# Performance work log

Measured on AMD Instinct MI355X. Metric: run time of the kernel, lower is better.

The kernel has to match this reference:

```python
import jax, jax.numpy as jnp
from jax import lax
import numpy as np


def _conv(x, w, b, pad):
    y = lax.conv_general_dilated(x, w, (1, 1), [(pad, pad), (pad, pad)],
                                 dimension_numbers=('NCHW', 'OIHW', 'NCHW'))
    return y + b[None, :, None, None]


def _bn(x, g, b, eps=1e-5):
    # training-mode batchnorm (batch statistics, biased variance) like torch default
    m = jnp.mean(x, (0, 2, 3), keepdims=True)
    v = jnp.mean((x - m) ** 2, (0, 2, 3), keepdims=True)
    return g[None, :, None, None] * (x - m) * lax.rsqrt(v + eps) + b[None, :, None, None]


def _maxpool2(x):
    return lax.reduce_window(x, -jnp.inf, lax.max, (1, 1, 2, 2), (1, 1, 2, 2), 'VALID')


def _power_features(x):
    # vectorized version of the per-image FFT + radial-bin histogram mean
    B, _, H, W = x.shape
    cy, cx = H // 2, W // 2
    yy, xx = jnp.meshgrid(jnp.arange(H), jnp.arange(W), indexing='ij')
    r = jnp.sqrt((xx - cx).astype(jnp.float32) ** 2 + (yy - cy).astype(jnp.float32) ** 2)
    max_r = min(H, W) // 2
    NB = 32
    r_bins = jnp.linspace(0.0, float(max_r), NB + 1)
    # bin j covers [r_bins[j], r_bins[j+1]) exactly as the torch mask
    idx = jnp.searchsorted(r_bins, r.ravel(), side='right') - 1
    valid = (idx >= 0) & (idx < NB)
    seg = jnp.where(valid, idx, NB)  # dump out-of-range into bin NB
    counts = jax.ops.segment_sum(valid.astype(jnp.float32), seg, NB + 1)[:NB]
    ps = jnp.abs(jnp.fft.fft2(x[:, 0])) ** 2  # [B,H,W]
    psf = ps.reshape(B, -1) * valid.astype(ps.dtype)[None, :]
    sums = jax.vmap(lambda p: jax.ops.segment_sum(p, seg, NB + 1))(psf)[:, :NB]
    radial = jnp.where(counts > 0, sums / jnp.maximum(counts, 1.0), 0.0)
    return jnp.log(radial + 1e-10)  # [B,32]


def reference(x, cw1, cb1, g1, bb1, cw2, cb2, g2, bb2, cw3, cb3, g3, bb3,
              cw4, cb4, g4, bb4, pcw, pcb, pg, pbb,
              pw1, pb1, pw2, pb2, pw3, pb3,
              fw1, fb1, fw2, fb2, fw3, fb3, fw4, fb4):
    h = jax.nn.relu(_bn(_conv(x, cw1, cb1, 2), g1, bb1)); h = _maxpool2(h)
    h = jax.nn.relu(_bn(_conv(h, cw2, cb2, 2), g2, bb2)); h = _maxpool2(h)
    h = jax.nn.relu(_bn(_conv(h, cw3, cb3, 1), g3, bb3)); h = _maxpool2(h)
    h = jax.nn.relu(_bn(_conv(h, cw4, cb4, 1), g4, bb4))        # [B,256,32,32]
    p = jax.nn.relu(_bn(_conv(h, pcw, pcb, 1), pg, pbb))        # [B,128,32,32]
    # adaptive avg pool (4,4): exact 8x8 windows, stride 8
    p = lax.reduce_window(p, 0.0, lax.add, (1, 1, 8, 8), (1, 1, 8, 8), 'VALID') / 64.0
    flat = p.reshape(p.shape[0], -1)  # [B,2048]
    pf = _power_features(x)           # [B,32]
    pf = jax.nn.relu(pf @ pw1.T + pb1)
    pf = jax.nn.relu(pf @ pw2.T + pb2)
    pf = jax.nn.relu(pf @ pw3.T + pb3)  # [B,64]
    c = jnp.concatenate([flat, pf], axis=1)  # [B,2112]
    c = jax.nn.relu(c @ fw1.T + fb1)
    c = jax.nn.relu(c @ fw2.T + fb2)
    c = jax.nn.relu(c @ fw3.T + fb3)
    return c @ fw4.T + fb4  # [B,2]


def setup_inputs() -> dict:
    key = jax.random.key(0)
    ki = iter(jax.random.split(key, 40))

    def W(shape):
        fan_in = int(np.prod(shape[1:]))
        return jax.random.normal(next(ki), shape, jnp.float32) / np.sqrt(fan_in)

    d = {'x': jax.random.normal(next(ki), (16, 1, 256, 256), jnp.float32)}
    convs = [('cw1', 'cb1', 'g1', 'bb1', (32, 1, 5, 5)),
             ('cw2', 'cb2', 'g2', 'bb2', (64, 32, 5, 5)),
             ('cw3', 'cb3', 'g3', 'bb3', (128, 64, 3, 3)),
             ('cw4', 'cb4', 'g4', 'bb4', (256, 128, 3, 3)),
             ('pcw', 'pcb', 'pg', 'pbb', (128, 256, 3, 3))]
    for wn, bn, gn, ben, s in convs:
        d[wn] = W(s); d[bn] = jnp.zeros(s[0], jnp.float32)
        d[gn] = jnp.ones(s[0], jnp.float32); d[ben] = jnp.zeros(s[0], jnp.float32)
    lins = [('pw1', 'pb1', (256, 32)), ('pw2', 'pb2', (128, 256)), ('pw3', 'pb3', (64, 128)),
            ('fw1', 'fb1', (512, 2112)), ('fw2', 'fb2', (256, 512)),
            ('fw3', 'fb3', (128, 256)), ('fw4', 'fb4', (2, 128))]
    for wn, bn, s in lins:
        d[wn] = W(s); d[bn] = jnp.zeros(s[0], jnp.float32)
    return d
```

## Files before the change

kernel.cpp:

```cpp
#include <hip/hip_runtime.h>
#include <math.h>


#define PI2F 6.283185307179586f

typedef _Float16 half8 __attribute__((ext_vector_type(8)));
typedef _Float16 half4v __attribute__((ext_vector_type(4)));
typedef float f32x4 __attribute__((ext_vector_type(4)));


__device__ __forceinline__ int bitrev8(int x) {
  x = ((x & 0x0F) << 4) | ((x >> 4) & 0x0F);
  x = ((x & 0x33) << 2) | ((x >> 2) & 0x33);
  x = ((x & 0x55) << 1) | ((x >> 1) & 0x55);
  return x;
}

__global__ __launch_bounds__(64)
void fft_rows(const float* __restrict__ x, float2* __restrict__ out) {
  __shared__ float2 s[256];
  __shared__ float2 tw[128];
  int blk = blockIdx.x;
  const float* rowp = x + (size_t)blk * 256;
  int t = threadIdx.x;
  for (int i = t; i < 128; i += 64) {
    float sn, cs;
    sincosf(-(PI2F / 256.f) * (float)i, &sn, &cs);
    tw[i] = make_float2(cs, sn);
  }
  #pragma unroll
  for (int e = 0; e < 4; ++e) {
    int i = t + (e << 6);
    s[bitrev8(i)] = make_float2(rowp[i], 0.f);
  }
  __syncthreads();
  #pragma unroll
  for (int st = 1; st <= 8; ++st) {
    int half = 1 << (st - 1);
    #pragma unroll
    for (int j = 0; j < 2; ++j) {
      int bf = t + (j << 6);
      int pos = bf & (half - 1);
      int grp = bf >> (st - 1);
      int i0 = (grp << st) | pos;
      int i1 = i0 + half;
      int k = pos << (8 - st);
      float cs = tw[k].x, sn = tw[k].y;
      float2 a = s[i0], b = s[i1];
      float tr = cs * b.x - sn * b.y;
      float ti = cs * b.y + sn * b.x;
      s[i0] = make_float2(a.x + tr, a.y + ti);
      s[i1] = make_float2(a.x - tr, a.y - ti);
    }
    __syncthreads();
  }
  float2* op = out + (size_t)blk * 256;
  #pragma unroll
  for (int e = 0; e < 4; ++e) { int i = t + (e << 6); op[i] = s[i]; }
}

__device__ __forceinline__ int radial_bin(int r2) {
  int j = (int)(sqrtf((float)r2) * 0.25f);
  while ((j + 1) * (j + 1) * 16 <= r2) ++j;
  while (j > 0 && j * j * 16 > r2) --j;
  return j;
}

__global__ __launch_bounds__(256)
void fft_cols_radial_v2(const float2* __restrict__ f, float* __restrict__ radial) {
  __shared__ float2 s[8][258];
  __shared__ float2 tw[128];
  __shared__ float bins[8][32];
  int b = blockIdx.x >> 5;
  int col0 = (blockIdx.x & 31) * 8;
  int t = threadIdx.x;
  for (int i = t; i < 128; i += 256) {
    float sn, cs;
    sincosf(-(PI2F / 256.f) * (float)i, &sn, &cs);
    tw[i] = make_float2(cs, sn);
  }
  ((float*)bins)[t] = 0.f;
  for (int idx = t; idx < 2048; idx += 256) {
    int row = idx >> 3, c = idx & 7;
    s[c][bitrev8(row)] = f[(size_t)b * 65536 + row * 256 + col0 + c];
  }
  __syncthreads();
  int c = t >> 5, l = t & 31;
  float2* sc = &s[c][0];
  #pragma unroll
  for (int st = 1; st <= 8; ++st) {
    int half = 1 << (st - 1);
    #pragma unroll
    for (int j = 0; j < 4; ++j) {
      int bf = l + (j << 5);
      int pos = bf & (half - 1);
      int grp = bf >> (st - 1);
      int i0 = (grp << st) | pos;
      int i1 = i0 + half;
      int k = pos << (8 - st);
      float cs = tw[k].x, sn = tw[k].y;
      float2 a = sc[i0], bb = sc[i1];
      float tr = cs * bb.x - sn * bb.y;
      float ti = cs * bb.y + sn * bb.x;
      sc[i0] = make_float2(a.x + tr, a.y + ti);
      sc[i1] = make_float2(a.x - tr, a.y - ti);
    }
    __syncthreads();
  }
  int dx = col0 + c - 128;
  #pragma unroll
  for (int e = 0; e < 8; ++e) {
    int i = l * 8 + e;
    float2 v = sc[i];
    float ps = v.x * v.x + v.y * v.y;
    int dy = i - 128;
    int r2 = dx * dx + dy * dy;
    if (r2 < 16384) atomicAdd(&bins[c][radial_bin(r2)], ps);
  }
  __syncthreads();
  if (t < 32) {
    float s0 = bins[0][t] + bins[1][t] + bins[2][t] + bins[3][t] +
               bins[4][t] + bins[5][t] + bins[6][t] + bins[7][t];
    atomicAdd(&radial[b * 32 + t], s0);
  }
}

__device__ __forceinline__ int isqrt_(int v) {
  int r = (int)sqrtf((float)v);
  while (r * r > v) --r;
  while ((r + 1) * (r + 1) <= v) ++r;
  return r;
}

__global__ __launch_bounds__(256)
void radial_finalize_v3(const float* __restrict__ radial, float* __restrict__ pf0) {
  __shared__ int red[4];
  __shared__ int cnt_s;
  int j = blockIdx.x, t = threadIdx.x;
  int dy = t - 128;
  int lo = 16 * j * j, hi = 16 * (j + 1) * (j + 1);
  int d2 = dy * dy;
  int cnt = 0;
  int tHi = hi - 1 - d2;
  if (tHi >= 0) {
    int rHi = isqrt_(tHi);
    int nHi = min(rHi, 127) + min(rHi, 128) + 1;
    int nLo = 0;
    int tLo = lo - 1 - d2;
    if (tLo >= 0) { int rLo = isqrt_(tLo); nLo = min(rLo, 127) + min(rLo, 128) + 1; }
    cnt = nHi - nLo;
  }
  #pragma unroll
  for (int off = 32; off > 0; off >>= 1) cnt += __shfl_down(cnt, off);
  if ((t & 63) == 0) red[t >> 6] = cnt;
  __syncthreads();
  if (t == 0) cnt_s = red[0] + red[1] + red[2] + red[3];
  __syncthreads();
  if (t < 16) {
    float cf = (float)cnt_s;
    float sum = radial[t * 32 + j];
    float val = cf > 0.f ? sum / fmaxf(cf, 1.f) : 0.f;
    pf0[t * 32 + j] = logf(val + 1e-10f);
  }
}


__global__ __launch_bounds__(256)
void wtrans_all(const float* __restrict__ cw2, const float* __restrict__ cw3,
                const float* __restrict__ cw4, const float* __restrict__ pcw,
                _Float16* __restrict__ wb2, _Float16* __restrict__ wb3,
                _Float16* __restrict__ wb4, _Float16* __restrict__ wbp) {
  int blk = blockIdx.x;
  const float* src; _Float16* dst; int COUT, CIN, KK, i;
  if (blk < 200)       { src = cw2; dst = wb2; COUT = 64;  CIN = 32;  KK = 25; i = blk * 256; }
  else if (blk < 488)  { src = cw3; dst = wb3; COUT = 128; CIN = 64;  KK = 9;  i = (blk - 200) * 256; }
  else if (blk < 1640) { src = cw4; dst = wb4; COUT = 256; CIN = 128; KK = 9;  i = (blk - 488) * 256; }
  else                 { src = pcw; dst = wbp; COUT = 128; CIN = 256; KK = 9;  i = (blk - 1640) * 256; }
  i += threadIdx.x;
  if (i >= COUT * CIN * KK) return;
  int ci = i % CIN;
  int r = i / CIN;
  int co = r % COUT;
  int tap = r / COUT;
  dst[i] = (_Float16)src[((size_t)co * CIN + ci) * KK + tap];
}


__device__ __forceinline__ void load16(float* d, const float* p) {
  f32x4 v0 = *(const f32x4*)(p);
  f32x4 v1 = *(const f32x4*)(p + 4);
  f32x4 v2 = *(const f32x4*)(p + 8);
  f32x4 v3 = *(const f32x4*)(p + 12);
  #pragma unroll
  for (int e = 0; e < 4; ++e) { d[e] = v0[e]; d[4+e] = v1[e]; d[8+e] = v2[e]; d[12+e] = v3[e]; }
}

__global__ __launch_bounds__(256)
void conv1_fused(const float* __restrict__ x, const float* __restrict__ w,
                 _Float16* __restrict__ praw, size_t minoff,
                 float* __restrict__ stats) {
  __shared__ float lds[8 * 264];
  __shared__ float r1[4][32], r2[4][32];
  int t = threadIdx.x;
  int y0 = blockIdx.x * 4, n = blockIdx.y;
  const float* xp = x + (size_t)n * 65536;
  for (int i = t; i < 8 * 264; i += 256) {
    int r = i / 264, cc = i % 264;
    int gy = y0 + r - 2, gx = cc - 4;
    lds[i] = (gy >= 0 && gy < 256 && gx >= 0 && gx < 256) ? xp[gy * 256 + gx] : 0.f;
  }
  __syncthreads();
  int c = t & 31, xg = t >> 5;
  float wreg[25];
  #pragma unroll
  for (int k = 0; k < 25; ++k) wreg[k] = w[c * 25 + k];
  float s1 = 0.f, s2 = 0.f;
  for (int strip = 0; strip < 4; ++strip) {
    int px0 = xg * 8 + strip * 64;
    float f[5][16];
    #pragma unroll
    for (int rr = 0; rr < 4; ++rr) load16(f[rr], &lds[rr * 264 + px0]);
    float pmax[4], pmin[4];
    #pragma unroll
    for (int r = 0; r < 4; ++r) {
      load16(f[(r + 4) % 5], &lds[(r + 4) * 264 + px0]);
      f32x4 A = {0.f, 0.f, 0.f, 0.f}, B = {0.f, 0.f, 0.f, 0.f};
      #pragma unroll
      for (int ky = 0; ky < 5; ++ky) {
        const float* fr = f[(r + ky) % 5];
        #pragma unroll
        for (int kx = 0; kx < 5; ++kx) {
          float wv = wreg[ky * 5 + kx];
          f32x4 ia = {fr[2 + kx], fr[3 + kx], fr[4 + kx], fr[5 + kx]};
          f32x4 ib = {fr[6 + kx], fr[7 + kx], fr[8 + kx], fr[9 + kx]};
          A += wv * ia; B += wv * ib;
        }
      }
      s1 += A[0] + A[1] + A[2] + A[3] + B[0] + B[1] + B[2] + B[3];
      s2 += A[0]*A[0] + A[1]*A[1] + A[2]*A[2] + A[3]*A[3]
          + B[0]*B[0] + B[1]*B[1] + B[2]*B[2] + B[3]*B[3];
      float cm[4], cn[4];
      cm[0] = fmaxf(A[0], A[1]); cn[0] = fminf(A[0], A[1]);
      cm[1] = fmaxf(A[2], A[3]); cn[1] = fminf(A[2], A[3]);
      cm[2] = fmaxf(B[0], B[1]); cn[2] = fminf(B[0], B[1]);
      cm[3] = fmaxf(B[2], B[3]); cn[3] = fminf(B[2], B[3]);
      if ((r & 1) == 0) {
        #pragma unroll
        for (int k = 0; k < 4; ++k) { pmax[k] = cm[k]; pmin[k] = cn[k]; }
      } else {
        int prow = (y0 + r) >> 1;
        int pc0 = px0 >> 1;
        #pragma unroll
        for (int k = 0; k < 4; ++k) {
          size_t idx = (((size_t)n * 128 + prow) * 128 + pc0 + k) * 32 + c;
          praw[idx] = (_Float16)fmaxf(pmax[k], cm[k]);
          praw[minoff + idx] = (_Float16)fminf(pmin[k], cn[k]);
        }
      }
    }
  }
  s1 += __shfl_down(s1, 32);
  s2 += __shfl_down(s2, 32);
  if ((t & 63) < 32) { r1[t >> 6][t & 31] = s1; r2[t >> 6][t & 31] = s2; }
  __syncthreads();
  if (t < 32) {
    float* st = stats + (blockIdx.x & 7) * 64;
    atomicAdd(&st[t],      r1[0][t] + r1[1][t] + r1[2][t] + r1[3][t]);
    atomicAdd(&st[32 + t], r2[0][t] + r2[1][t] + r2[2][t] + r2[3][t]);
  }
}


__global__ __launch_bounds__(256)
void bn_apply(const _Float16* __restrict__ raw, size_t minoff,
              const float* __restrict__ stats, const float* __restrict__ g,
              const float* __restrict__ bb, _Float16* __restrict__ out,
              int C, int HWC, float invN) {
  __shared__ float scs[64], shs[64];
  int t = threadIdx.x, n = blockIdx.y;
  for (int c = t; c < C; c += 256) {
    float s1 = 0.f, s2 = 0.f;
    #pragma unroll
    for (int s = 0; s < 8; ++s) {
      s1 += stats[s * 2 * C + c];
      s2 += stats[s * 2 * C + C + c];
    }
    float mean = s1 * invN;
    float var  = s2 * invN - mean * mean;
    float k = g[c] / sqrtf(var + 1e-5f);
    scs[c] = k; shs[c] = bb[c] - mean * k;
  }
  __syncthreads();
  size_t basei = (size_t)n * HWC;
  int nv = HWC >> 3;
  for (int i = blockIdx.x * 256 + t; i < nv; i += gridDim.x * 256) {
    size_t off = basei + ((size_t)i << 3);
    half8 vmx = *(const half8*)(raw + off);
    half8 vmn = *(const half8*)(raw + minoff + off);
    int ch = (i << 3) & (C - 1);
    half8 o;
    #pragma unroll
    for (int j = 0; j < 8; ++j) {
      float sc = scs[ch + j];
      float xv = sc >= 0.f ? (float)vmx[j] : (float)vmn[j];
      o[j] = (_Float16)fmaxf(sc * xv + shs[ch + j], 0.f);
    }
    *(half8*)(out + off) = o;
  }
}


template <int CIN, int COUT, int H, int W, int K, int TH, int TW, int CW,
          int COT, int PT, int SLAB, int APPLY, int INPOOL, int OUTPOOL>
__global__ __launch_bounds__(256)
void conv_mfma5(const _Float16* __restrict__ in, size_t in_minoff,
                const _Float16* __restrict__ wb,
                _Float16* __restrict__ out, size_t out_minoff,
                const float* __restrict__ instats, const float* __restrict__ ing,
                const float* __restrict__ inbb, float in_invN,
                float* __restrict__ stats) {
  constexpr int P = K / 2, R = TH + 2 * P, XW = TW + 2 * P, PIX = R * XW;
  constexpr int TAPS = K * K, CSP = SLAB + 8;
  constexpr int NCC = SLAB / 32, NPH = CIN / SLAB, SUBS = SLAB / 8;
  constexpr int PW = 4 / CW, COB = CW * 16 * COT;
  static_assert(TH * TW == PW * 16 * PT, "pos tile mismatch");
  static_assert(TW == 16, "row-per-fragment requires TW=16");
  static_assert(!OUTPOOL || (PT % 2 == 0), "pool needs even PT");
  __shared__ _Float16 lds[PIX * CSP];
  __shared__ float inscs[APPLY ? CIN : 8], inshs[APPLY ? CIN : 8];
  __shared__ float sst[2][COB];
  int t = threadIdx.x;
  int lane = t & 63, wv = t >> 6;
  int lane15 = lane & 15, quad = lane >> 4;
  constexpr int WT = W / TW;
  int x0 = (blockIdx.x % WT) * TW, y0 = (blockIdx.x / WT) * TH;
  int coB = blockIdx.y * COB;
  int nb = blockIdx.z;
  int co_off = (wv % CW) * (16 * COT);
  int rowbase = (wv / CW) * PT;

  for (int i = t; i < 2 * COB; i += 256) ((float*)sst)[i] = 0.f;
  if (APPLY) {
    for (int c = t; c < CIN; c += 256) {
      float s1 = 0.f, s2 = 0.f;
      #pragma unroll
      for (int s = 0; s < 8; ++s) {
        s1 += instats[s * 2 * CIN + c];
        s2 += instats[s * 2 * CIN + CIN + c];
      }
      float mean = s1 * in_invN;
      float var  = s2 * in_invN - mean * mean;
      float k = ing[c] / sqrtf(var + 1e-5f);
      inscs[c] = k; inshs[c] = inbb[c] - mean * k;
    }
    __syncthreads();
  }

  f32x4 acc[COT][PT];
  #pragma unroll
  for (int ct = 0; ct < COT; ++ct)
    #pragma unroll
    for (int pt = 0; pt < PT; ++pt)
      #pragma unroll
      for (int e = 0; e < 4; ++e) acc[ct][pt][e] = 0.f;

  int bbase[PT];
  #pragma unroll
  for (int pt = 0; pt < PT; ++pt)
    bbase[pt] = ((rowbase + pt) * XW + lane15) * CSP + quad * 8;
  const _Float16* aptr[COT];
  #pragma unroll
  for (int ct = 0; ct < COT; ++ct)
    aptr[ct] = wb + (size_t)(coB + co_off + ct * 16 + lane15) * CIN + quad * 8;

  const size_t ibase = (size_t)nb * H * W * CIN;

  #pragma unroll
  for (int ph = 0; ph < NPH; ++ph) {
    constexpr int ITEMS = PIX * SUBS;
    for (int i = t; i < ITEMS; i += 256) {
      int sub = i % SUBS, pix = i / SUBS;
      int r = pix / XW, xx = pix % XW;
      int gy = y0 + r - P, gx = x0 + xx - P;
      int ch = ph * SLAB + sub * 8;
      half8 v;
      #pragma unroll
      for (int j = 0; j < 8; ++j) v[j] = (_Float16)0.f;
      if (gy >= 0 && gy < H && gx >= 0 && gx < W) {
        size_t off = ibase + ((size_t)gy * W + gx) * CIN + ch;
        half8 vmx = *(const half8*)(in + off);
        if (!APPLY) {
          v = vmx;
        } else if (INPOOL) {
          half8 vmn = *(const half8*)(in + in_minoff + off);
          #pragma unroll
          for (int j = 0; j < 8; ++j) {
            float sc = inscs[ch + j];
            float xv = sc >= 0.f ? (float)vmx[j] : (float)vmn[j];
            v[j] = (_Float16)fmaxf(sc * xv + inshs[ch + j], 0.f);
          }
        } else {
          #pragma unroll
          for (int j = 0; j < 8; ++j) {
            float sc = inscs[ch + j];
            v[j] = (_Float16)fmaxf(sc * (float)vmx[j] + inshs[ch + j], 0.f);
          }
        }
      }
      *(half8*)(&lds[pix * CSP + sub * 8]) = v;
    }
    __syncthreads();
    #pragma unroll
    for (int cc = 0; cc < NCC; ++cc) {
      #pragma unroll
      for (int tap = 0; tap < TAPS; ++tap) {
        int ky = tap / K, kx = tap % K;
        half8 a[COT], b[PT];
        #pragma unroll
        for (int ct = 0; ct < COT; ++ct)
          a[ct] = *(const half8*)(aptr[ct] + (size_t)tap * COUT * CIN +
                                  ph * SLAB + cc * 32);
        #pragma unroll
        for (int pt = 0; pt < PT; ++pt)
          b[pt] = *(const half8*)(&lds[bbase[pt] + (ky * XW + kx) * CSP + cc * 32]);
        #pragma unroll
        for (int ct = 0; ct < COT; ++ct)
          #pragma unroll
          for (int pt = 0; pt < PT; ++pt)
            acc[ct][pt] = __builtin_amdgcn_mfma_f32_16x16x32_f16(
                a[ct], b[pt], acc[ct][pt], 0, 0, 0);
      }
    }
    if (ph + 1 < NPH) __syncthreads();
  }

  if (OUTPOOL) {
    #pragma unroll
    for (int ct = 0; ct < COT; ++ct)
      #pragma unroll
      for (int pp = 0; pp < PT; pp += 2) {
        half4v hmax, hmin;
        #pragma unroll
        for (int e = 0; e < 4; ++e) {
          float vmx = fmaxf(acc[ct][pp][e], acc[ct][pp + 1][e]);
          float vmn = fminf(acc[ct][pp][e], acc[ct][pp + 1][e]);
          float omx = fmaxf(vmx, __shfl_xor(vmx, 1));
          float omn = fminf(vmn, __shfl_xor(vmn, 1));
          hmax[e] = (_Float16)omx; hmin[e] = (_Float16)omn;
        }
        if ((lane15 & 1) == 0) {
          int co = coB + co_off + ct * 16 + quad * 4;
          int prow = (y0 + rowbase + pp) >> 1;
          int pcol = (x0 >> 1) + (lane15 >> 1);
          size_t idx = (((size_t)nb * (H / 2) + prow) * (W / 2) + pcol) * COUT + co;
          *(half4v*)(out + idx) = hmax;
          *(half4v*)(out + out_minoff + idx) = hmin;
        }
      }
  } else {
    #pragma unroll
    for (int ct = 0; ct < COT; ++ct)
      #pragma unroll
      for (int pt = 0; pt < PT; ++pt) {
        int co = coB + co_off + ct * 16 + quad * 4;
        int y = y0 + rowbase + pt, x = x0 + lane15;
        _Float16* op = out + (((size_t)nb * H + y) * W + x) * COUT + co;
        half4v h;
        #pragma unroll
        for (int e = 0; e < 4; ++e) h[e] = (_Float16)acc[ct][pt][e];
        *(half4v*)op = h;
      }
  }

  #pragma unroll
  for (int ct = 0; ct < COT; ++ct)
    #pragma unroll
    for (int e = 0; e < 4; ++e) {
      float sv = 0.f, sq = 0.f;
      #pragma unroll
      for (int pt = 0; pt < PT; ++pt) {
        float v = acc[ct][pt][e];
        sv += v; sq += v * v;
      }
      sv += __shfl_xor(sv, 1); sq += __shfl_xor(sq, 1);
      sv += __shfl_xor(sv, 2); sq += __shfl_xor(sq, 2);
      sv += __shfl_xor(sv, 4); sq += __shfl_xor(sq, 4);
      sv += __shfl_xor(sv, 8); sq += __shfl_xor(sq, 8);
      if (lane15 == 0) {
        int cl = co_off + ct * 16 + quad * 4 + e;
        atomicAdd(&sst[0][cl], sv);
        atomicAdd(&sst[1][cl], sq);
      }
    }
  __syncthreads();
  float* st = stats + (blockIdx.x & 7) * 2 * COUT;
  for (int i = t; i < COB; i += 256) {
    atomicAdd(&st[coB + i], sst[0][i]);
    atomicAdd(&st[COUT + coB + i], sst[1][i]);
  }
}


__global__ __launch_bounds__(256)
void bn_avgpool_concat(const _Float16* __restrict__ x, const float* __restrict__ stats,
                       const float* __restrict__ g, const float* __restrict__ bb,
                       float* __restrict__ concat, float invN) {
  __shared__ float scs[128], shs[128];
  int t = threadIdx.x;
  int n = blockIdx.y;
  for (int c = t; c < 128; c += 256) {
    float s1 = 0.f, s2 = 0.f;
    #pragma unroll
    for (int s = 0; s < 8; ++s) {
      s1 += stats[s * 256 + c];
      s2 += stats[s * 256 + 128 + c];
    }
    float mean = s1 * invN;
    float var  = s2 * invN - mean * mean;
    float k = g[c] / sqrtf(var + 1e-5f);
    scs[c] = k; shs[c] = bb[c] - mean * k;
  }
  __syncthreads();
  int i = blockIdx.x * 256 + t;
  int c = i & 127, opix = i >> 7;
  int py = opix >> 2, px = opix & 3;
  float sc = scs[c], sh = shs[c];
  float s = 0.f;
  for (int yy = 0; yy < 8; ++yy)
    #pragma unroll
    for (int xx = 0; xx < 8; ++xx)
      s += fmaxf((float)x[(((size_t)n * 32 + py * 8 + yy) * 32 + px * 8 + xx) * 128 + c] * sc + sh, 0.f);
  concat[(size_t)n * 2112 + c * 16 + opix] = s * (1.f / 64.f);
}


__global__ __launch_bounds__(64)
void linear_k(const float* __restrict__ in, const float* __restrict__ w,
              const float* __restrict__ bias, float* __restrict__ out,
              int I, int in_stride, int out_stride, int relu) {
  int o = blockIdx.x, b = blockIdx.y;
  int lane = threadIdx.x;
  const float* ip = in + (size_t)b * in_stride;
  const float* wp = w + (size_t)o * I;
  float acc = 0.f;
  for (int i = lane; i < I; i += 64) acc += ip[i] * wp[i];
  #pragma unroll
  for (int off = 32; off > 0; off >>= 1) acc += __shfl_down(acc, off);
  if (lane == 0) {
    float v = acc + bias[o];
    if (relu) v = fmaxf(v, 0.f);
    out[(size_t)b * out_stride + o] = v;
  }
}

__global__ __launch_bounds__(256)
void pf_mlp(const float* __restrict__ pf0,
            const float* __restrict__ pw1, const float* __restrict__ pb1,
            const float* __restrict__ pw2, const float* __restrict__ pb2,
            const float* __restrict__ pw3, const float* __restrict__ pb3,
            float* __restrict__ concat) {
  __shared__ float a0[32], a1[256], a2[128];
  int b = blockIdx.x, t = threadIdx.x;
  if (t < 32) a0[t] = pf0[b * 32 + t];
  __syncthreads();
  {
    float s = pb1[t];
    for (int i = 0; i < 32; ++i) s += pw1[t * 32 + i] * a0[i];
    a1[t] = fmaxf(s, 0.f);
  }
  __syncthreads();
  if (t < 128) {
    float s = pb2[t];
    for (int i = 0; i < 256; ++i) s += pw2[t * 256 + i] * a1[i];
    a2[t] = fmaxf(s, 0.f);
  }
  __syncthreads();
  if (t < 64) {
    float s = pb3[t];
    for (int i = 0; i < 128; ++i) s += pw3[t * 128 + i] * a2[i];
    concat[(size_t)b * 2112 + 2048 + t] = fmaxf(s, 0.f);
  }
}

__global__ __launch_bounds__(256)
void fc_tail(const float* __restrict__ fc1o,
             const float* __restrict__ fw2, const float* __restrict__ fb2,
             const float* __restrict__ fw3, const float* __restrict__ fb3,
             const float* __restrict__ fw4, const float* __restrict__ fb4,
             float* __restrict__ out) {
  __shared__ float a1[512], a2[256], a3[128];
  int b = blockIdx.x, t = threadIdx.x;
  a1[t] = fc1o[b * 512 + t];
  a1[t + 256] = fc1o[b * 512 + t + 256];
  __syncthreads();
  {
    float s = fb2[t];
    for (int i = 0; i < 512; ++i) s += fw2[t * 512 + i] * a1[i];
    a2[t] = fmaxf(s, 0.f);
  }
  __syncthreads();
  if (t < 128) {
    float s = fb3[t];
    for (int i = 0; i < 256; ++i) s += fw3[t * 256 + i] * a2[i];
    a3[t] = fmaxf(s, 0.f);
  }
  __syncthreads();
  if (t < 2) {
    float s = fb4[t];
    for (int i = 0; i < 128; ++i) s += fw4[t * 128 + i] * a3[i];
    out[b * 2 + t] = s;
  }
}


extern "C" void kernel_launch(void* const* d_in, const int* in_sizes, int n_in,
                              void* d_out, int out_size, void* d_ws, size_t ws_size,
                              hipStream_t stream) {
  (void)in_sizes; (void)n_in; (void)out_size; (void)ws_size;
  const float* x   = (const float*)d_in[0];
  const float* cw1 = (const float*)d_in[1];
  const float* g1  = (const float*)d_in[3];
  const float* bb1 = (const float*)d_in[4];
  const float* cw2 = (const float*)d_in[5];
  const float* g2  = (const float*)d_in[7];
  const float* bb2 = (const float*)d_in[8];
  const float* cw3 = (const float*)d_in[9];
  const float* g3  = (const float*)d_in[11];
  const float* bb3 = (const float*)d_in[12];
  const float* cw4 = (const float*)d_in[13];
  const float* g4  = (const float*)d_in[15];
  const float* bb4 = (const float*)d_in[16];
  const float* pcw = (const float*)d_in[17];
  const float* pg  = (const float*)d_in[19];
  const float* pbb = (const float*)d_in[20];
  const float* pw1 = (const float*)d_in[21];
  const float* pb1 = (const float*)d_in[22];
  const float* pw2 = (const float*)d_in[23];
  const float* pb2 = (const float*)d_in[24];
  const float* pw3 = (const float*)d_in[25];
  const float* pb3 = (const float*)d_in[26];
  const float* fw1 = (const float*)d_in[27];
  const float* fb1 = (const float*)d_in[28];
  const float* fw2 = (const float*)d_in[29];
  const float* fb2 = (const float*)d_in[30];
  const float* fw3 = (const float*)d_in[31];
  const float* fb3 = (const float*)d_in[32];
  const float* fw4 = (const float*)d_in[33];
  const float* fb4 = (const float*)d_in[34];

  char* base = (char*)d_ws;
  float2*   fftbuf   = (float2*)(base + 0);
  _Float16* pool1raw = (_Float16*)(base + 0);
  _Float16* pool1app = (_Float16*)(base + 33554432);
  _Float16* pool2raw = (_Float16*)(base + 0);
  _Float16* pool2app = (_Float16*)(base + 16777216);
  _Float16* pool3raw = (_Float16*)(base + 0);
  _Float16* conv4raw = (_Float16*)(base + 8388608);
  _Float16* pconvo   = (_Float16*)(base + 16777216);
  _Float16* wb2      = (_Float16*)(base + 50331648);
  _Float16* wb3      = (_Float16*)(base + 50434048);
  _Float16* wb4      = (_Float16*)(base + 50581504);
  _Float16* wbp      = (_Float16*)(base + 51171328);
  float*    zbase    = (float*)(base + 51761152);
  float*    stats1   = zbase;
  float*    stats2   = zbase + 512;
  float*    stats3   = zbase + 1536;
  float*    stats4   = zbase + 3584;
  float*    stats5   = zbase + 7680;
  float*    radial   = zbase + 9728;
  float*    pf0      = (float*)(base + 51802112);
  float*    concat   = (float*)(base + 51804160);
  float*    fc1o     = (float*)(base + 51939328);

  hipMemsetAsync(zbase, 0, 10240 * sizeof(float), stream);

  wtrans_all<<<2792, 256, 0, stream>>>(cw2, cw3, cw4, pcw, wb2, wb3, wb4, wbp);

  fft_rows<<<4096, 64, 0, stream>>>(x, fftbuf);
  fft_cols_radial_v2<<<512, 256, 0, stream>>>(fftbuf, radial);
  radial_finalize_v3<<<32, 256, 0, stream>>>(radial, pf0);
  pf_mlp<<<16, 256, 0, stream>>>(pf0, pw1, pb1, pw2, pb2, pw3, pb3, concat);

  conv1_fused<<<dim3(64, 16), 256, 0, stream>>>(x, cw1, pool1raw, 8388608, stats1);
  bn_apply<<<dim3(128, 16), 256, 0, stream>>>(
      pool1raw, 8388608, stats1, g1, bb1, pool1app, 32, 524288, 1.f / 1048576.f);

  conv_mfma5<32, 64, 128, 128, 5, 4, 16, 2, 2, 2, 32, 0, 0, 1>
      <<<dim3(256, 1, 16), 256, 0, stream>>>(
      pool1app, 0, wb2, pool2raw, 4194304,
      nullptr, nullptr, nullptr, 0.f, stats2);
  bn_apply<<<dim3(128, 16), 256, 0, stream>>>(
      pool2raw, 4194304, stats2, g2, bb2, pool2app, 64, 262144, 1.f / 262144.f);

  conv_mfma5<64, 128, 64, 64, 3, 4, 16, 2, 2, 2, 64, 0, 0, 1>
      <<<dim3(64, 2, 16), 256, 0, stream>>>(
      pool2app, 0, wb3, pool3raw, 2097152,
      nullptr, nullptr, nullptr, 0.f, stats3);

  conv_mfma5<128, 256, 32, 32, 3, 4, 16, 2, 2, 2, 128, 1, 1, 0>
      <<<dim3(16, 4, 16), 256, 0, stream>>>(
      pool3raw, 2097152, wb4, conv4raw, 0,
      stats3, g3, bb3, 1.f / 65536.f, stats4);

  conv_mfma5<256, 128, 32, 32, 3, 4, 16, 2, 2, 2, 128, 1, 0, 0>
      <<<dim3(16, 2, 16), 256, 0, stream>>>(
      conv4raw, 0, wbp, pconvo, 0,
      stats4, g4, bb4, 1.f / 16384.f, stats5);
  bn_avgpool_concat<<<dim3(8, 16), 256, 0, stream>>>(
      pconvo, stats5, pg, pbb, concat, 1.f / 16384.f);

  linear_k<<<dim3(512, 16), 64, 0, stream>>>(concat, fw1, fb1, fc1o, 2112, 2112, 512, 1);
  fc_tail<<<16, 256, 0, stream>>>(fc1o, fw2, fb2, fw3, fb3, fw4, fb4, (float*)d_out);
}
```

Baseline: 434.0 us.

## Use 32x32 MFMA for conv2/conv3 and split stats, BN+pool into passes

Adds a conv kernel built on the 32x32x16 MFMA instruction for conv2 and conv3. It writes full-resolution fp16 outputs with no fused pooling or statistics. A separate stats_pass computes the batchnorm sums, and a new bn_applypool kernel fuses BN, ReLU and 2x2 max-pool, replacing the earlier max/min dual-buffer pooling scheme. Conv4 now reads the already-normalized pooled input instead of applying BN on the fly. The larger MFMA tiles are meant to raise matrix throughput, but the change adds extra full-resolution memory traffic and more kernel launches.

```diff
diff --git a/kernel.cpp b/kernel.cpp
--- a/kernel.cpp
+++ b/kernel.cpp
@@ -7,6 +7,7 @@
 typedef _Float16 half8 __attribute__((ext_vector_type(8)));
 typedef _Float16 half4v __attribute__((ext_vector_type(4)));
 typedef float f32x4 __attribute__((ext_vector_type(4)));
+typedef float f32x16 __attribute__((ext_vector_type(16)));
 
 
 __device__ __forceinline__ int bitrev8(int x) {
@@ -271,6 +272,21 @@
 }
 
 
+__device__ __forceinline__ void bn_coeff(const float* stats, int C, int c,
+                                         float invN, const float* g,
+                                         const float* bb, float* sc, float* sh) {
+  float s1 = 0.f, s2 = 0.f;
+  #pragma unroll
+  for (int s = 0; s < 8; ++s) {
+    s1 += stats[s * 2 * C + c];
+    s2 += stats[s * 2 * C + C + c];
+  }
+  float mean = s1 * invN;
+  float var  = s2 * invN - mean * mean;
+  float k = g[c] / sqrtf(var + 1e-5f);
+  *sc = k; *sh = bb[c] - mean * k;
+}
+
 __global__ __launch_bounds__(256)
 void bn_apply(const _Float16* __restrict__ raw, size_t minoff,
               const float* __restrict__ stats, const float* __restrict__ g,
@@ -278,18 +294,7 @@
               int C, int HWC, float invN) {
   __shared__ float scs[64], shs[64];
   int t = threadIdx.x, n = blockIdx.y;
-  for (int c = t; c < C; c += 256) {
-    float s1 = 0.f, s2 = 0.f;
-    #pragma unroll
-    for (int s = 0; s < 8; ++s) {
-      s1 += stats[s * 2 * C + c];
-      s2 += stats[s * 2 * C + C + c];
-    }
-    float mean = s1 * invN;
-    float var  = s2 * invN - mean * mean;
-    float k = g[c] / sqrtf(var + 1e-5f);
-    scs[c] = k; shs[c] = bb[c] - mean * k;
-  }
+  for (int c = t; c < C; c += 256) bn_coeff(stats, C, c, invN, g, bb, &scs[c], &shs[c]);
   __syncthreads();
   size_t basei = (size_t)n * HWC;
   int nv = HWC >> 3;
@@ -306,6 +311,163 @@
       o[j] = (_Float16)fmaxf(sc * xv + shs[ch + j], 0.f);
     }
     *(half8*)(out + off) = o;
+  }
+}
+
+
+template <int CIN, int COUT, int H, int W, int K, int COT, int SLAB>
+__global__ __launch_bounds__(256)
+void conv_mfma32(const _Float16* __restrict__ in, const _Float16* __restrict__ wb,
+                 _Float16* __restrict__ out) {
+  constexpr int P = K / 2, TH = 8, TW = 16, R = TH + 2 * P, XW = TW + 2 * P;
+  constexpr int PIX = R * XW, TAPS = K * K, CSP = SLAB + 8;
+  constexpr int NCC = SLAB / 16, NPH = CIN / SLAB, SUBS = SLAB / 8;
+  constexpr int COB = 32 * COT;
+  __shared__ _Float16 lds[PIX * CSP];
+  int t = threadIdx.x;
+  int lane = t & 63, wv = t >> 6;
+  int n31 = lane & 31, khalf = lane >> 5;
+  constexpr int WT = W / TW;
+  int x0 = (blockIdx.x % WT) * TW, y0 = (blockIdx.x / WT) * TH;
+  int coB = blockIdx.y * COB;
+  int nb = blockIdx.z;
+  int rowbase = wv * 2;
+
+  f32x16 acc[COT];
+  #pragma unroll
+  for (int ct = 0; ct < COT; ++ct)
+    #pragma unroll
+    for (int e = 0; e < 16; ++e) acc[ct][e] = 0.f;
+
+  int bbase = ((rowbase + (n31 >> 4)) * XW + (n31 & 15)) * CSP + khalf * 8;
+  const _Float16* aptr[COT];
+  #pragma unroll
+  for (int ct = 0; ct < COT; ++ct)
+    aptr[ct] = wb + (size_t)(coB + ct * 32 + n31) * CIN + khalf * 8;
+
+  const size_t ibase = (size_t)nb * H * W * CIN;
+
+  #pragma unroll
+  for (int ph = 0; ph < NPH; ++ph) {
+    constexpr int ITEMS = PIX * SUBS;
+    for (int i = t; i < ITEMS; i += 256) {
+      int sub = i % SUBS, pix = i / SUBS;
+      int r = pix / XW, xx = pix % XW;
+      int gy = y0 + r - P, gx = x0 + xx - P;
+      half8 v;
+      #pragma unroll
+      for (int j = 0; j < 8; ++j) v[j] = (_Float16)0.f;
+      if (gy >= 0 && gy < H && gx >= 0 && gx < W)
+        v = *(const half8*)(in + ibase + ((size_t)gy * W + gx) * CIN +
+                            ph * SLAB + sub * 8);
+      *(half8*)(&lds[pix * CSP + sub * 8]) = v;
+    }
+    __syncthreads();
+    #pragma unroll
+    for (int cc = 0; cc < NCC; ++cc) {
+      #pragma unroll
+      for (int tap = 0; tap < TAPS; ++tap) {
+        int ky = tap / K, kx = tap % K;
+        half8 b = *(const half8*)(&lds[bbase + (ky * XW + kx) * CSP + cc * 16]);
+        #pragma unroll
+        for (int ct = 0; ct < COT; ++ct) {
+          half8 a = *(const half8*)(aptr[ct] + (size_t)tap * COUT * CIN +
+                                    ph * SLAB + cc * 16);
+          acc[ct] = __builtin_amdgcn_mfma_f32_32x32x16_f16(a, b, acc[ct], 0, 0, 0);
+        }
+      }
+    }
+    if (ph + 1 < NPH) __syncthreads();
+  }
+
+  int y = y0 + rowbase + (n31 >> 4), x = x0 + (n31 & 15);
+  _Float16* op = out + (((size_t)nb * H + y) * W + x) * COUT;
+  #pragma unroll
+  for (int ct = 0; ct < COT; ++ct)
+    #pragma unroll
+    for (int g = 0; g < 4; ++g) {
+      half4v h;
+      #pragma unroll
+      for (int e = 0; e < 4; ++e) h[e] = (_Float16)acc[ct][g * 4 + e];
+      *(half4v*)(op + coB + ct * 32 + 8 * g + 4 * khalf) = h;
+    }
+}
+
+
+template <int C>
+__global__ __launch_bounds__(256)
+void stats_pass(const _Float16* __restrict__ x, float* __restrict__ stats,
+                int HW) {
+  constexpr int CT = C / 8;
+  constexpr int PPB = 256 / CT;
+  __shared__ float red[256][16];
+  int t = threadIdx.x, n = blockIdx.y;
+  int cb = (t % CT) * 8, pr = t / CT;
+  int chunk = HW / 8;
+  int p0 = blockIdx.x * chunk;
+  float s[8], q[8];
+  #pragma unroll
+  for (int j = 0; j < 8; ++j) { s[j] = 0.f; q[j] = 0.f; }
+  const _Float16* xp = x + (size_t)n * HW * C;
+  for (int p = p0 + pr; p < p0 + chunk; p += PPB) {
+    half8 v = *(const half8*)(xp + (size_t)p * C + cb);
+    #pragma unroll
+    for (int j = 0; j < 8; ++j) { float f = (float)v[j]; s[j] += f; q[j] += f * f; }
+  }
+  #pragma unroll
+  for (int j = 0; j < 8; ++j) { red[t][j] = s[j]; red[t][8 + j] = q[j]; }
+  __syncthreads();
+  for (int st = 128; st >= CT; st >>= 1) {
+    if (t < st)
+      #pragma unroll
+      for (int j = 0; j < 16; ++j) red[t][j] += red[t + st][j];
+    __syncthreads();
+  }
+  if (t < CT) {
+    float* sl = stats + (blockIdx.x & 7) * 2 * C;
+    #pragma unroll
+    for (int j = 0; j < 8; ++j) {
+      atomicAdd(&sl[t * 8 + j], red[t][j]);
+      atomicAdd(&sl[C + t * 8 + j], red[t][8 + j]);
+    }
+  }
+}
+
+
+template <int C>
+__global__ __launch_bounds__(256)
+void bn_applypool(const _Float16* __restrict__ raw, const float* __restrict__ stats,
+                  const float* __restrict__ g, const float* __restrict__ bb,
+                  _Float16* __restrict__ out, int H, int W, float invN) {
+  constexpr int CT = C / 8;
+  __shared__ float scs[C], shs[C];
+  int t = threadIdx.x, n = blockIdx.y;
+  for (int c = t; c < C; c += 256) bn_coeff(stats, C, c, invN, g, bb, &scs[c], &shs[c]);
+  __syncthreads();
+  int W2 = W >> 1, H2 = H >> 1;
+  int total = H2 * W2 * CT;
+  const _Float16* xp = raw + (size_t)n * H * W * C;
+  _Float16* op = out + (size_t)n * H2 * W2 * C;
+  for (int i = blockIdx.x * 256 + t; i < total; i += gridDim.x * 256) {
+    int cb = (i % CT) * 8;
+    int pp = i / CT;
+    int py = pp / W2, px = pp % W2;
+    const _Float16* p00 = xp + ((size_t)(2 * py) * W + 2 * px) * C + cb;
+    half8 v00 = *(const half8*)(p00);
+    half8 v01 = *(const half8*)(p00 + C);
+    half8 v10 = *(const half8*)(p00 + (size_t)W * C);
+    half8 v11 = *(const half8*)(p00 + (size_t)W * C + C);
+    half8 o;
+    #pragma unroll
+    for (int j = 0; j < 8; ++j) {
+      float sc = scs[cb + j], sh = shs[cb + j];
+      float a = fmaxf(sc * (float)v00[j] + sh, 0.f);
+      float b = fmaxf(sc * (float)v01[j] + sh, 0.f);
+      float d = fmaxf(sc * (float)v10[j] + sh, 0.f);
+      float e = fmaxf(sc * (float)v11[j] + sh, 0.f);
+      o[j] = (_Float16)fmaxf(fmaxf(a, b), fmaxf(d, e));
+    }
+    *(half8*)(op + (size_t)pp * C + cb) = o;
   }
 }
 
@@ -325,7 +487,6 @@
   constexpr int PW = 4 / CW, COB = CW * 16 * COT;
   static_assert(TH * TW == PW * 16 * PT, "pos tile mismatch");
   static_assert(TW == 16, "row-per-fragment requires TW=16");
-  static_assert(!OUTPOOL || (PT % 2 == 0), "pool needs even PT");
   __shared__ _Float16 lds[PIX * CSP];
   __shared__ float inscs[APPLY ? CIN : 8], inshs[APPLY ? CIN : 8];
   __shared__ float sst[2][COB];
@@ -341,18 +502,8 @@
 
   for (int i = t; i < 2 * COB; i += 256) ((float*)sst)[i] = 0.f;
   if (APPLY) {
-    for (int c = t; c < CIN; c += 256) {
-      float s1 = 0.f, s2 = 0.f;
-      #pragma unroll
-      for (int s = 0; s < 8; ++s) {
-        s1 += instats[s * 2 * CIN + c];
-        s2 += instats[s * 2 * CIN + CIN + c];
-      }
-      float mean = s1 * in_invN;
-      float var  = s2 * in_invN - mean * mean;
-      float k = ing[c] / sqrtf(var + 1e-5f);
-      inscs[c] = k; inshs[c] = inbb[c] - mean * k;
-    }
+    for (int c = t; c < CIN; c += 256)
+      bn_coeff(instats, CIN, c, in_invN, ing, inbb, &inscs[c], &inshs[c]);
     __syncthreads();
   }
 
@@ -434,43 +585,18 @@
     if (ph + 1 < NPH) __syncthreads();
   }
 
-  if (OUTPOOL) {
-    #pragma unroll
-    for (int ct = 0; ct < COT; ++ct)
-      #pragma unroll
-      for (int pp = 0; pp < PT; pp += 2) {
-        half4v hmax, hmin;
-        #pragma unroll
-        for (int e = 0; e < 4; ++e) {
-          float vmx = fmaxf(acc[ct][pp][e], acc[ct][pp + 1][e]);
-          float vmn = fminf(acc[ct][pp][e], acc[ct][pp + 1][e]);
-          float omx = fmaxf(vmx, __shfl_xor(vmx, 1));
-          float omn = fminf(vmn, __shfl_xor(vmn, 1));
-          hmax[e] = (_Float16)omx; hmin[e] = (_Float16)omn;
-        }
-        if ((lane15 & 1) == 0) {
-          int co = coB + co_off + ct * 16 + quad * 4;
-          int prow = (y0 + rowbase + pp) >> 1;
-          int pcol = (x0 >> 1) + (lane15 >> 1);
-          size_t idx = (((size_t)nb * (H / 2) + prow) * (W / 2) + pcol) * COUT + co;
-          *(half4v*)(out + idx) = hmax;
-          *(half4v*)(out + out_minoff + idx) = hmin;
-        }
-      }
-  } else {
-    #pragma unroll
-    for (int ct = 0; ct < COT; ++ct)
-      #pragma unroll
-      for (int pt = 0; pt < PT; ++pt) {
-        int co = coB + co_off + ct * 16 + quad * 4;
-        int y = y0 + rowbase + pt, x = x0 + lane15;
-        _Float16* op = out + (((size_t)nb * H + y) * W + x) * COUT + co;
-        half4v h;
-        #pragma unroll
-        for (int e = 0; e < 4; ++e) h[e] = (_Float16)acc[ct][pt][e];
-        *(half4v*)op = h;
-      }
-  }
+  #pragma unroll
+  for (int ct = 0; ct < COT; ++ct)
+    #pragma unroll
+    for (int pt = 0; pt < PT; ++pt) {
+      int co = coB + co_off + ct * 16 + quad * 4;
+      int y = y0 + rowbase + pt, x = x0 + lane15;
+      _Float16* op = out + (((size_t)nb * H + y) * W + x) * COUT + co;
+      half4v h;
+      #pragma unroll
+      for (int e = 0; e < 4; ++e) h[e] = (_Float16)acc[ct][pt][e];
+      *(half4v*)op = h;
+    }
 
   #pragma unroll
   for (int ct = 0; ct < COT; ++ct)
@@ -508,18 +634,7 @@
   __shared__ float scs[128], shs[128];
   int t = threadIdx.x;
   int n = blockIdx.y;
-  for (int c = t; c < 128; c += 256) {
-    float s1 = 0.f, s2 = 0.f;
-    #pragma unroll
-    for (int s = 0; s < 8; ++s) {
-      s1 += stats[s * 256 + c];
-      s2 += stats[s * 256 + 128 + c];
-    }
-    float mean = s1 * invN;
-    float var  = s2 * invN - mean * mean;
-    float k = g[c] / sqrtf(var + 1e-5f);
-    scs[c] = k; shs[c] = bb[c] - mean * k;
-  }
+  for (int c = t; c < 128; c += 256) bn_coeff(stats, 128, c, invN, g, bb, &scs[c], &shs[c]);
   __syncthreads();
   int i = blockIdx.x * 256 + t;
   int c = i & 127, opix = i >> 7;
@@ -651,12 +766,13 @@
   char* base = (char*)d_ws;
   float2*   fftbuf   = (float2*)(base + 0);
   _Float16* pool1raw = (_Float16*)(base + 0);
+  _Float16* conv2o   = (_Float16*)(base + 0);
+  _Float16* conv3o   = (_Float16*)(base + 0);
+  _Float16* conv4raw = (_Float16*)(base + 0);
+  _Float16* pconvo   = (_Float16*)(base + 8388608);
   _Float16* pool1app = (_Float16*)(base + 33554432);
-  _Float16* pool2raw = (_Float16*)(base + 0);
-  _Float16* pool2app = (_Float16*)(base + 16777216);
-  _Float16* pool3raw = (_Float16*)(base + 0);
-  _Float16* conv4raw = (_Float16*)(base + 8388608);
-  _Float16* pconvo   = (_Float16*)(base + 16777216);
+  _Float16* pool2app = (_Float16*)(base + 33554432);
+  _Float16* pool3app = (_Float16*)(base + 33554432);
   _Float16* wb2      = (_Float16*)(base + 50331648);
   _Float16* wb3      = (_Float16*)(base + 50434048);
   _Float16* wb4      = (_Float16*)(base + 50581504);
@@ -685,22 +801,22 @@
   bn_apply<<<dim3(128, 16), 256, 0, stream>>>(
       pool1raw, 8388608, stats1, g1, bb1, pool1app, 32, 524288, 1.f / 1048576.f);
 
-  conv_mfma5<32, 64, 128, 128, 5, 4, 16, 2, 2, 2, 32, 0, 0, 1>
-      <<<dim3(256, 1, 16), 256, 0, stream>>>(
-      pool1app, 0, wb2, pool2raw, 4194304,
-      nullptr, nullptr, nullptr, 0.f, stats2);
-  bn_apply<<<dim3(128, 16), 256, 0, stream>>>(
-      pool2raw, 4194304, stats2, g2, bb2, pool2app, 64, 262144, 1.f / 262144.f);
-
-  conv_mfma5<64, 128, 64, 64, 3, 4, 16, 2, 2, 2, 64, 0, 0, 1>
-      <<<dim3(64, 2, 16), 256, 0, stream>>>(
-      pool2app, 0, wb3, pool3raw, 2097152,
-      nullptr, nullptr, nullptr, 0.f, stats3);
-
-  conv_mfma5<128, 256, 32, 32, 3, 4, 16, 2, 2, 2, 128, 1, 1, 0>
+  conv_mfma32<32, 64, 128, 128, 5, 2, 32><<<dim3(128, 1, 16), 256, 0, stream>>>(
+      pool1app, wb2, conv2o);
+  stats_pass<64><<<dim3(8, 16), 256, 0, stream>>>(conv2o, stats2, 16384);
+  bn_applypool<64><<<dim3(32, 16), 256, 0, stream>>>(
+      conv2o, stats2, g2, bb2, pool2app, 128, 128, 1.f / 262144.f);
+
+  conv_mfma32<64, 128, 64, 64, 3, 2, 64><<<dim3(32, 2, 16), 256, 0, stream>>>(
+      pool2app, wb3, conv3o);
+  stats_pass<128><<<dim3(8, 16), 256, 0, stream>>>(conv3o, stats3, 4096);
+  bn_applypool<128><<<dim3(16, 16), 256, 0, stream>>>(
+      conv3o, stats3, g3, bb3, pool3app, 64, 64, 1.f / 65536.f);
+
+  conv_mfma5<128, 256, 32, 32, 3, 4, 16, 2, 2, 2, 128, 0, 0, 0>
       <<<dim3(16, 4, 16), 256, 0, stream>>>(
-      pool3raw, 2097152, wb4, conv4raw, 0,
-      stats3, g3, bb3, 1.f / 65536.f, stats4);
+      pool3app, 0, wb4, conv4raw, 0,
+      nullptr, nullptr, nullptr, 0.f, stats4);
 
   conv_mfma5<256, 128, 32, 32, 3, 4, 16, 2, 2, 2, 128, 1, 0, 0>
       <<<dim3(16, 2, 16), 256, 0, stream>>>(
```

Measured after the change: 475.9 us. 1.1x slower.
